# Kernel tuning notes

Measured on AMD Instinct MI355X. Metric: run time of the kernel, lower is better.

Reference implementation:

```python
import jax, jax.numpy as jnp
import numpy as np

B = 64
L_IN = 4001
L_CONV = 998  # (4001-10)//4 + 1
D = 1000
EPS = 1e-5


def _convlin(x, cw, cb, lw, lb):
    # x: (B,1,4001), cw: (1,1,10), lw: (1000,998)
    y = jax.lax.conv_general_dilated(
        x, cw, window_strides=(4,), padding='VALID',
        dimension_numbers=('NCH', 'OIH', 'NCH')) + cb[None, :, None]  # (B,1,998)
    y = y @ lw.T + lb  # (B,1,1000)
    return jax.nn.relu(y)


def setup_inputs() -> dict:
    key = jax.random.key(0)
    ks = jax.random.split(key, 24)
    f32 = jnp.float32
    inp = {
        'x': jax.random.normal(ks[0], (B, 1, L_IN), dtype=f32),
        'bn_gamma': jnp.ones((L_IN,), f32),
        'bn_beta': jnp.zeros((L_IN,), f32),
        'bn_mean': jax.random.normal(ks[1], (L_IN,), f32) * 0.1,
        'bn_var': jax.random.uniform(ks[2], (L_IN,), f32, 0.5, 1.5),
        'conv_w_q': jax.random.normal(ks[3], (1, 1, 10), f32) * 0.3,
        'conv_b_q': jax.random.normal(ks[4], (1,), f32) * 0.1,
        'lin_w_q': jax.random.normal(ks[5], (D, L_CONV), f32) * (1.0 / np.sqrt(L_CONV)),
        'lin_b_q': jax.random.normal(ks[6], (D,), f32) * 0.02,
        'conv_w_k': jax.random.normal(ks[7], (1, 1, 10), f32) * 0.3,
        'conv_b_k': jax.random.normal(ks[8], (1,), f32) * 0.1,
        'lin_w_k': jax.random.normal(ks[9], (D, L_CONV), f32) * (1.0 / np.sqrt(L_CONV)),
        'lin_b_k': jax.random.normal(ks[10], (D,), f32) * 0.02,
        'conv_w_v': jax.random.normal(ks[11], (1, 1, 10), f32) * 0.3,
        'conv_b_v': jax.random.normal(ks[12], (1,), f32) * 0.1,
        'lin_w_v': jax.random.normal(ks[13], (D, L_CONV), f32) * (1.0 / np.sqrt(L_CONV)),
        'lin_b_v': jax.random.normal(ks[14], (D,), f32) * 0.02,
        'in_proj_w': jax.random.normal(ks[15], (3, 1), f32),
        'in_proj_b': jax.random.normal(ks[16], (3,), f32) * 0.02,
        'out_proj_w': jax.random.normal(ks[17], (1, 1), f32),
        'out_proj_b': jax.random.normal(ks[18], (1,), f32) * 0.02,
        'out_w': jax.random.normal(ks[19], (D, D), f32) * (1.0 / np.sqrt(D)),
        'out_b': jax.random.normal(ks[20], (D,), f32) * 0.02,
    }
    return inp


def reference(x, bn_gamma, bn_beta, bn_mean, bn_var,
              conv_w_q, conv_b_q, lin_w_q, lin_b_q,
              conv_w_k, conv_b_k, lin_w_k, lin_b_k,
              conv_w_v, conv_b_v, lin_w_v, lin_b_v,
              in_proj_w, in_proj_b, out_proj_w, out_proj_b,
              out_w, out_b):
    # BatchNorm1d over last dim (eval mode, running stats); x: (B,1,4001)
    xn = (x - bn_mean[None, None, :]) * jax.lax.rsqrt(bn_var[None, None, :] + EPS)
    xn = xn * bn_gamma[None, None, :] + bn_beta[None, None, :]

    Q = _convlin(xn, conv_w_q, conv_b_q, lin_w_q, lin_b_q)[:, 0, :]  # (B,1000)
    K = _convlin(xn, conv_w_k, conv_b_k, lin_w_k, lin_b_k)[:, 0, :]
    V = _convlin(xn, conv_w_v, conv_b_v, lin_w_v, lin_b_v)[:, 0, :]

    # MHA with embed_dim=1, num_heads=1 -> scalar in-projections, scale = 1
    q = Q * in_proj_w[0, 0] + in_proj_b[0]  # (B,1000)
    k = K * in_proj_w[1, 0] + in_proj_b[1]
    v = V * in_proj_w[2, 0] + in_proj_b[2]

    scores = q[:, :, None] * k[:, None, :]  # (B,1000,1000)
    attn = jax.nn.softmax(scores, axis=-1)
    ctx = jnp.einsum('bqk,bk->bq', attn, v)  # (B,1000)
    ctx = ctx * out_proj_w[0, 0] + out_proj_b[0]

    out = ctx[:, None, :] @ out_w.T + out_b  # (B,1,1000)
    return out
```

## Files before the change

### kernel.cpp

```cpp
#include <hip/hip_runtime.h>
#include <math.h>

#define NB 64
#define LIN 4001
#define LC 998
#define ND 1000
#define EPSBN 1e-5f

#define CK 96
#define NCH_LIN 11
#define NCH_OUT 11

#define OFF_CONVT 0u
#define OFF_PP    191616u
#define OFF_Q     2354304u
#define OFF_KV    2418304u
#define OFF_CF    2549376u
#define OFF_OP    2613376u

__global__ __launch_bounds__(256) void k_bnconv(
    const float* __restrict__ x,
    const float* __restrict__ g, const float* __restrict__ be,
    const float* __restrict__ mu, const float* __restrict__ va,
    const float* __restrict__ cwq, const float* __restrict__ cbq,
    const float* __restrict__ cwk, const float* __restrict__ cbk,
    const float* __restrict__ cwv, const float* __restrict__ cbv,
    float* __restrict__ convT)
{
    int j = blockIdx.x * 256 + threadIdx.x;
    int b = blockIdx.y;
    if (j >= LC) return;
    const float* xb = x + (size_t)b * LIN + 4 * j;
    float aq = 0.f, ak = 0.f, av = 0.f;
#pragma unroll
    for (int t = 0; t < 10; ++t) {
        int i = 4 * j + t;
        float s  = g[i] * rsqrtf(va[i] + EPSBN);
        float xn = (xb[t] - mu[i]) * s + be[i];
        aq = fmaf(xn, cwq[t], aq);
        ak = fmaf(xn, cwk[t], ak);
        av = fmaf(xn, cwv[t], av);
    }
    convT[((size_t)0 * LC + j) * 64 + b] = aq + cbq[0];
    convT[((size_t)1 * LC + j) * 64 + b] = ak + cbk[0];
    convT[((size_t)2 * LC + j) * 64 + b] = av + cbv[0];
}

__device__ __forceinline__ void gemm_tile(
    const float* __restrict__ Asrc,
    const float* __restrict__ Brow,
    int ldB, int dgb, int j0, int jc,
    float* __restrict__ Pt,
    float* lds)
{
    float* ldsC = lds;
    float* ldsW = lds + 6144;
    int tid  = threadIdx.x;
    int lane = tid & 63;
    int w    = tid >> 6;
    int b0   = (lane & 7) << 3;
    int d0   = (lane >> 3) << 3;

    {
        const float4* src = (const float4*)Asrc;
        float4* dst = (float4*)ldsC;
        for (int t = tid; t < jc * 16; t += 256) dst[t] = src[t];
    }
    for (int idx = tid; idx < 3072; idx += 256) {
        int dd = idx / 48, j2 = idx % 48;
        int dg = dgb + dd;
        float2 v = make_float2(0.f, 0.f);
        if (dg < ND && 2 * j2 < jc)
            v = *(const float2*)(Brow + (size_t)dg * ldB + j0 + 2 * j2);
        ldsW[dd * 97 + 2 * j2]     = v.x;
        ldsW[dd * 97 + 2 * j2 + 1] = v.y;
    }
    __syncthreads();

    float acc[8][8];
#pragma unroll
    for (int i = 0; i < 8; ++i)
#pragma unroll
        for (int jx = 0; jx < 8; ++jx) acc[i][jx] = 0.f;

    int js = (jc * w) >> 2;
    int je = (jc * (w + 1)) >> 2;
    for (int jj = js; jj < je; ++jj) {
        float4 c0 = *(const float4*)(ldsC + jj * 64 + b0);
        float4 c1 = *(const float4*)(ldsC + jj * 64 + b0 + 4);
        float cv[8] = {c0.x, c0.y, c0.z, c0.w, c1.x, c1.y, c1.z, c1.w};
        float wv[8];
#pragma unroll
        for (int r = 0; r < 8; ++r) wv[r] = ldsW[(d0 + r) * 97 + jj];
#pragma unroll
        for (int i = 0; i < 8; ++i)
#pragma unroll
            for (int jx = 0; jx < 8; ++jx)
                acc[i][jx] = fmaf(cv[i], wv[jx], acc[i][jx]);
    }
    __syncthreads();

    for (int p = 0; p < 2; ++p) {
        float* red = lds + w * 2304;
#pragma unroll
        for (int i = 0; i < 8; ++i)
            *(float4*)(red + (b0 + i) * 36 + (d0 >> 1)) =
                make_float4(acc[i][4*p], acc[i][4*p+1], acc[i][4*p+2], acc[i][4*p+3]);
        __syncthreads();
        for (int t = tid; t < 512; t += 256) {
            int bb = t >> 3, gg = t & 7;
            int o = bb * 36 + 4 * gg;
            float4 a0 = *(const float4*)(lds + o);
            float4 a1 = *(const float4*)(lds + 2304 + o);
            float4 a2 = *(const float4*)(lds + 4608 + o);
            float4 a3 = *(const float4*)(lds + 6912 + o);
            float4 s;
            s.x = a0.x + a1.x + a2.x + a3.x;
            s.y = a0.y + a1.y + a2.y + a3.y;
            s.z = a0.z + a1.z + a2.z + a3.z;
            s.w = a0.w + a1.w + a2.w + a3.w;
            *(float4*)(Pt + bb * 64 + 8 * gg + 4 * p) = s;
        }
        __syncthreads();
    }
}

__global__ __launch_bounds__(256) void k_lin(
    const float* __restrict__ convT,
    const float* __restrict__ lwq, const float* __restrict__ lwk,
    const float* __restrict__ lwv,
    float* __restrict__ Pp)
{
    __shared__ float lds[12352];
    int dgb   = blockIdx.x * 64;
    int which = blockIdx.y;
    int chunk = blockIdx.z;
    int j0 = chunk * CK;
    int jc = (LC - j0 < CK) ? (LC - j0) : CK;
    const float* lw = (which == 0) ? lwq : ((which == 1) ? lwk : lwv);
    const float* Asrc = convT + ((size_t)which * LC + j0) * 64;
    float* Pt = Pp + (((size_t)chunk * 3 + which) * 16 + blockIdx.x) * 4096;
    gemm_tile(Asrc, lw, LC, dgb, j0, jc, Pt, lds);
}

__global__ __launch_bounds__(256) void k_act(
    const float* __restrict__ Pp,
    const float* __restrict__ lbq, const float* __restrict__ lbk,
    const float* __restrict__ lbv,
    const float* __restrict__ ipw, const float* __restrict__ ipb,
    float* __restrict__ q, float* __restrict__ kv)
{
    int i = blockIdx.x * 256 + threadIdx.x;
    int b = blockIdx.y;
    if (i >= ND) return;
    int it = i >> 6, il = i & 63;
    float s0 = 0.f, s1 = 0.f, s2 = 0.f;
    for (int c = 0; c < NCH_LIN; ++c) {
        size_t base = (((size_t)c * 3) * 16 + it) * 4096 + (il | (b << 6));
        s0 += Pp[base];
        s1 += Pp[base + 16 * 4096];
        s2 += Pp[base + 32 * 4096];
    }
    float yq = fmaxf(s0 + lbq[i], 0.f) * ipw[0] + ipb[0];
    float yk = fmaxf(s1 + lbk[i], 0.f) * ipw[1] + ipb[1];
    float yv = fmaxf(s2 + lbv[i], 0.f) * ipw[2] + ipb[2];
    q[(size_t)b * ND + i] = yq;
    kv[(size_t)b * 2048 + 2 * i]     = yk;
    kv[(size_t)b * 2048 + 2 * i + 1] = yv;
}

__global__ __launch_bounds__(256) void k_attn(
    const float* __restrict__ q, const float* __restrict__ kv,
    const float* __restrict__ opw, const float* __restrict__ opb,
    float* __restrict__ cfT)
{
    __shared__ float ldsKV[2048];
    __shared__ float sden[256];
    __shared__ float snum[256];
    __shared__ float rmax[4];
    __shared__ float rmin[4];
    int tid = threadIdx.x;
    int b   = blockIdx.y;
    int w   = tid >> 6;
    int ii  = tid & 63;
    int i   = blockIdx.x * 64 + ii;

    {
        const float4* src = (const float4*)(kv + (size_t)b * 2048);
        float4* dst = (float4*)ldsKV;
        for (int t = tid; t < 512; t += 256) dst[t] = src[t];
    }
    __syncthreads();

    const float2* kv2 = (const float2*)ldsKV;
    float km = -INFINITY, kn = INFINITY;
    for (int idx = tid; idx < ND; idx += 256) {
        float2 f = kv2[idx];
        km = fmaxf(km, f.x);
        kn = fminf(kn, f.x);
    }
#pragma unroll
    for (int off = 1; off < 64; off <<= 1) {
        km = fmaxf(km, __shfl_xor(km, off));
        kn = fminf(kn, __shfl_xor(kn, off));
    }
    if (ii == 0) { rmax[w] = km; rmin[w] = kn; }
    __syncthreads();
    km = fmaxf(fmaxf(rmax[0], rmax[1]), fmaxf(rmax[2], rmax[3]));
    kn = fminf(fminf(rmin[0], rmin[1]), fminf(rmin[2], rmin[3]));

    float qi = (i < ND) ? q[(size_t)b * ND + i] : 0.f;
    float m  = (qi >= 0.f) ? qi * km : qi * kn;

    int jb = w * 250;
    float den = 0.f, num = 0.f;
#pragma unroll 2
    for (int jl = 0; jl < 250; ++jl) {
        float2 f = kv2[jb + jl];
        float e  = __expf(fmaf(qi, f.x, -m));
        den += e;
        num = fmaf(e, f.y, num);
    }
    sden[tid] = den;
    snum[tid] = num;
    __syncthreads();
    if (w == 0 && i < ND) {
        float dt = sden[ii] + sden[64 + ii] + sden[128 + ii] + sden[192 + ii];
        float nt = snum[ii] + snum[64 + ii] + snum[128 + ii] + snum[192 + ii];
        cfT[(size_t)i * 64 + b] = (nt / dt) * opw[0] + opb[0];
    }
}

__global__ __launch_bounds__(256) void k_out(
    const float* __restrict__ cfT, const float* __restrict__ W,
    float* __restrict__ Op)
{
    __shared__ float lds[12352];
    int egb   = blockIdx.x * 64;
    int chunk = blockIdx.y;
    int j0 = chunk * CK;
    int jc = (ND - j0 < CK) ? (ND - j0) : CK;
    const float* Asrc = cfT + (size_t)j0 * 64;
    float* Pt = Op + ((size_t)chunk * 16 + blockIdx.x) * 4096;
    gemm_tile(Asrc, W, ND, egb, j0, jc, Pt, lds);
}

__global__ __launch_bounds__(256) void k_fin(
    const float* __restrict__ Op, const float* __restrict__ outb,
    float* __restrict__ out)
{
    int e = blockIdx.x * 256 + threadIdx.x;
    int b = blockIdx.y;
    if (e >= ND) return;
    float s = outb[e];
    size_t cell = ((size_t)(e >> 6)) * 4096 + (b << 6) + (e & 63);
    for (int c = 0; c < NCH_OUT; ++c)
        s += Op[(size_t)c * 16 * 4096 + cell];
    out[(size_t)b * ND + e] = s;
}

extern "C" void kernel_launch(void* const* d_in, const int* in_sizes, int n_in,
                              void* d_out, int out_size, void* d_ws, size_t ws_size,
                              hipStream_t stream)
{
    const float* x    = (const float*)d_in[0];
    const float* g    = (const float*)d_in[1];
    const float* be   = (const float*)d_in[2];
    const float* mu   = (const float*)d_in[3];
    const float* va   = (const float*)d_in[4];
    const float* cwq  = (const float*)d_in[5];
    const float* cbq  = (const float*)d_in[6];
    const float* lwq  = (const float*)d_in[7];
    const float* lbq  = (const float*)d_in[8];
    const float* cwk  = (const float*)d_in[9];
    const float* cbk  = (const float*)d_in[10];
    const float* lwk  = (const float*)d_in[11];
    const float* lbk  = (const float*)d_in[12];
    const float* cwv  = (const float*)d_in[13];
    const float* cbv  = (const float*)d_in[14];
    const float* lwv  = (const float*)d_in[15];
    const float* lbv  = (const float*)d_in[16];
    const float* ipw  = (const float*)d_in[17];
    const float* ipb  = (const float*)d_in[18];
    const float* opw  = (const float*)d_in[19];
    const float* opb  = (const float*)d_in[20];
    const float* W    = (const float*)d_in[21];
    const float* outb = (const float*)d_in[22];

    float* ws    = (float*)d_ws;
    float* convT = ws + OFF_CONVT;
    float* Pp    = ws + OFF_PP;
    float* q     = ws + OFF_Q;
    float* kv    = ws + OFF_KV;
    float* cfT   = ws + OFF_CF;
    float* Op    = ws + OFF_OP;
    float* out   = (float*)d_out;

    k_bnconv<<<dim3(4, 64), 256, 0, stream>>>(x, g, be, mu, va,
                                              cwq, cbq, cwk, cbk, cwv, cbv, convT);
    k_lin  <<<dim3(16, 3, NCH_LIN), 256, 0, stream>>>(convT, lwq, lwk, lwv, Pp);
    k_act  <<<dim3(4, 64), 256, 0, stream>>>(Pp, lbq, lbk, lbv, ipw, ipb, q, kv);
    k_attn <<<dim3(16, 64), 256, 0, stream>>>(q, kv, opw, opb, cfT);
    k_out  <<<dim3(16, NCH_OUT), 256, 0, stream>>>(cfT, W, Op);
    k_fin  <<<dim3(4, 64), 256, 0, stream>>>(Op, outb, out);
}
```

Measured before the change: 166.3 us.

## Fuse split-K reduction and activation into attention kernel, two queries per thread

Removes the separate k_act kernel. The attention kernel now reduces the split-K partial sums for K, V and Q itself, applies bias, ReLU and the in-projection, and writes K/V into LDS. Each block handles 128 queries, two per thread, so each K/V load from LDS is reused twice. Pre-scaling K by log2(e) lets the loop use exp2f. This drops one launch and a global round trip, but the K/V reduction is now repeated by each of the 8 blocks per batch row.

```diff
diff --git a/kernel.cpp b/kernel.cpp
--- a/kernel.cpp
+++ b/kernel.cpp
@@ -13,10 +13,8 @@
 
 #define OFF_CONVT 0u
 #define OFF_PP    191616u
-#define OFF_Q     2354304u
-#define OFF_KV    2418304u
-#define OFF_CF    2549376u
-#define OFF_OP    2613376u
+#define OFF_CF    2354304u
+#define OFF_OP    2418304u
 
 __global__ __launch_bounds__(256) void k_bnconv(
     const float* __restrict__ x,
@@ -143,91 +141,101 @@
     gemm_tile(Asrc, lw, LC, dgb, j0, jc, Pt, lds);
 }
 
-__global__ __launch_bounds__(256) void k_act(
+__global__ __launch_bounds__(256) void k_attn(
     const float* __restrict__ Pp,
     const float* __restrict__ lbq, const float* __restrict__ lbk,
     const float* __restrict__ lbv,
     const float* __restrict__ ipw, const float* __restrict__ ipb,
-    float* __restrict__ q, float* __restrict__ kv)
-{
-    int i = blockIdx.x * 256 + threadIdx.x;
-    int b = blockIdx.y;
-    if (i >= ND) return;
-    int it = i >> 6, il = i & 63;
-    float s0 = 0.f, s1 = 0.f, s2 = 0.f;
-    for (int c = 0; c < NCH_LIN; ++c) {
-        size_t base = (((size_t)c * 3) * 16 + it) * 4096 + (il | (b << 6));
-        s0 += Pp[base];
-        s1 += Pp[base + 16 * 4096];
-        s2 += Pp[base + 32 * 4096];
-    }
-    float yq = fmaxf(s0 + lbq[i], 0.f) * ipw[0] + ipb[0];
-    float yk = fmaxf(s1 + lbk[i], 0.f) * ipw[1] + ipb[1];
-    float yv = fmaxf(s2 + lbv[i], 0.f) * ipw[2] + ipb[2];
-    q[(size_t)b * ND + i] = yq;
-    kv[(size_t)b * 2048 + 2 * i]     = yk;
-    kv[(size_t)b * 2048 + 2 * i + 1] = yv;
-}
-
-__global__ __launch_bounds__(256) void k_attn(
-    const float* __restrict__ q, const float* __restrict__ kv,
     const float* __restrict__ opw, const float* __restrict__ opb,
     float* __restrict__ cfT)
 {
-    __shared__ float ldsKV[2048];
-    __shared__ float sden[256];
-    __shared__ float snum[256];
+    __shared__ float skv[2000];
+    __shared__ float sql[128];
+    __shared__ float sd[512];
+    __shared__ float sn[512];
     __shared__ float rmax[4];
     __shared__ float rmin[4];
-    int tid = threadIdx.x;
-    int b   = blockIdx.y;
-    int w   = tid >> 6;
-    int ii  = tid & 63;
-    int i   = blockIdx.x * 64 + ii;
-
-    {
-        const float4* src = (const float4*)(kv + (size_t)b * 2048);
-        float4* dst = (float4*)ldsKV;
-        for (int t = tid; t < 512; t += 256) dst[t] = src[t];
-    }
-    __syncthreads();
-
-    const float2* kv2 = (const float2*)ldsKV;
+    const float LOG2E = 1.4426950408889634f;
+    int tid  = threadIdx.x;
+    int b    = blockIdx.y;
+    int i0   = blockIdx.x * 128;
+    int w    = tid >> 6;
+    int lane = tid & 63;
+
+    float ipw1 = ipw[1], ipb1 = ipb[1];
+    float ipw2 = ipw[2], ipb2 = ipb[2];
+
+    for (int j = tid; j < ND; j += 256) {
+        int it = j >> 6, il = j & 63;
+        size_t base = ((size_t)it) * 4096 + (b << 6) + il;
+        float sk = 0.f, sv = 0.f;
+        for (int c = 0; c < NCH_LIN; ++c) {
+            sk += Pp[((size_t)(c * 3 + 1) * 16) * 4096 + base];
+            sv += Pp[((size_t)(c * 3 + 2) * 16) * 4096 + base];
+        }
+        float yk = fmaxf(sk + lbk[j], 0.f) * ipw1 + ipb1;
+        float yv = fmaxf(sv + lbv[j], 0.f) * ipw2 + ipb2;
+        skv[2 * j]     = yk * LOG2E;
+        skv[2 * j + 1] = yv;
+    }
+    if (tid < 128) {
+        int i = i0 + tid;
+        float sq = 0.f;
+        if (i < ND) {
+            int it = i >> 6, il = i & 63;
+            size_t base = ((size_t)it) * 4096 + (b << 6) + il;
+            for (int c = 0; c < NCH_LIN; ++c)
+                sq += Pp[((size_t)(c * 3 + 0) * 16) * 4096 + base];
+            sq = fmaxf(sq + lbq[i], 0.f) * ipw[0] + ipb[0];
+        }
+        sql[tid] = sq;
+    }
+    __syncthreads();
+
     float km = -INFINITY, kn = INFINITY;
-    for (int idx = tid; idx < ND; idx += 256) {
-        float2 f = kv2[idx];
-        km = fmaxf(km, f.x);
-        kn = fminf(kn, f.x);
+    for (int j = tid; j < ND; j += 256) {
+        float f = skv[2 * j];
+        km = fmaxf(km, f);
+        kn = fminf(kn, f);
     }
 #pragma unroll
     for (int off = 1; off < 64; off <<= 1) {
         km = fmaxf(km, __shfl_xor(km, off));
         kn = fminf(kn, __shfl_xor(kn, off));
     }
-    if (ii == 0) { rmax[w] = km; rmin[w] = kn; }
+    if (lane == 0) { rmax[w] = km; rmin[w] = kn; }
     __syncthreads();
     km = fmaxf(fmaxf(rmax[0], rmax[1]), fmaxf(rmax[2], rmax[3]));
     kn = fminf(fminf(rmin[0], rmin[1]), fminf(rmin[2], rmin[3]));
 
-    float qi = (i < ND) ? q[(size_t)b * ND + i] : 0.f;
-    float m  = (qi >= 0.f) ? qi * km : qi * kn;
-
+    float q0 = sql[lane];
+    float q1 = sql[64 + lane];
+    float m0 = (q0 >= 0.f) ? q0 * km : q0 * kn;
+    float m1 = (q1 >= 0.f) ? q1 * km : q1 * kn;
+    const float2* kv2 = (const float2*)skv;
     int jb = w * 250;
-    float den = 0.f, num = 0.f;
+    float d0a = 0.f, n0a = 0.f, d1a = 0.f, n1a = 0.f;
 #pragma unroll 2
     for (int jl = 0; jl < 250; ++jl) {
         float2 f = kv2[jb + jl];
-        float e  = __expf(fmaf(qi, f.x, -m));
-        den += e;
-        num = fmaf(e, f.y, num);
-    }
-    sden[tid] = den;
-    snum[tid] = num;
-    __syncthreads();
-    if (w == 0 && i < ND) {
-        float dt = sden[ii] + sden[64 + ii] + sden[128 + ii] + sden[192 + ii];
-        float nt = snum[ii] + snum[64 + ii] + snum[128 + ii] + snum[192 + ii];
-        cfT[(size_t)i * 64 + b] = (nt / dt) * opw[0] + opb[0];
+        float e0 = exp2f(fmaf(q0, f.x, -m0));
+        float e1 = exp2f(fmaf(q1, f.x, -m1));
+        d0a += e0; n0a = fmaf(e0, f.y, n0a);
+        d1a += e1; n1a = fmaf(e1, f.y, n1a);
+    }
+    sd[w * 128 + lane]      = d0a;
+    sd[w * 128 + 64 + lane] = d1a;
+    sn[w * 128 + lane]      = n0a;
+    sn[w * 128 + 64 + lane] = n1a;
+    __syncthreads();
+
+    if (tid < 128) {
+        int i = i0 + tid;
+        if (i < ND) {
+            float dt = sd[tid] + sd[128 + tid] + sd[256 + tid] + sd[384 + tid];
+            float nt = sn[tid] + sn[128 + tid] + sn[256 + tid] + sn[384 + tid];
+            cfT[(size_t)i * 64 + b] = (nt / dt) * opw[0] + opb[0];
+        }
     }
 }
 
@@ -290,8 +298,6 @@
     float* ws    = (float*)d_ws;
     float* convT = ws + OFF_CONVT;
     float* Pp    = ws + OFF_PP;
-    float* q     = ws + OFF_Q;
-    float* kv    = ws + OFF_KV;
     float* cfT   = ws + OFF_CF;
     float* Op    = ws + OFF_OP;
     float* out   = (float*)d_out;
@@ -299,8 +305,8 @@
     k_bnconv<<<dim3(4, 64), 256, 0, stream>>>(x, g, be, mu, va,
                                               cwq, cbq, cwk, cbk, cwv, cbv, convT);
     k_lin  <<<dim3(16, 3, NCH_LIN), 256, 0, stream>>>(convT, lwq, lwk, lwv, Pp);
-    k_act  <<<dim3(4, 64), 256, 0, stream>>>(Pp, lbq, lbk, lbv, ipw, ipb, q, kv);
-    k_attn <<<dim3(16, 64), 256, 0, stream>>>(q, kv, opw, opb, cfT);
+    k_attn <<<dim3(8, 64), 256, 0, stream>>>(Pp, lbq, lbk, lbv, ipw, ipb,
+                                             opw, opb, cfT);
     k_out  <<<dim3(16, NCH_OUT), 256, 0, stream>>>(cfT, W, Op);
     k_fin  <<<dim3(4, 64), 256, 0, stream>>>(Op, outb, out);
 }
```

New measurement: 174.5 us. 4.9% more time.

## Stream GEMM operands from global memory and retile K chunks with padded conv buffer

Applied to the files above, without the earlier changes.

Both linear GEMMs (the Q/K/V projections and the output projection) drop LDS staging of the convolution activations and weight tiles. Each thread now reads its 8 weight rows as float2 and its activations as float4 straight from global memory. The convT buffer is padded to 1024 zero-filled columns, and the K-chunk sizes change to 128 and 64, with a 3-blocks-per-CU occupancy hint. The softmax switches to exp2f with log2(e) folded into K during activation. Removing the row guard on weight loads means tail blocks read past the last weight row, which risks out-of-bounds access. Per-thread global loads also rely on the cache hierarchy for reuse.

```diff
diff --git a/kernel.cpp b/kernel.cpp
--- a/kernel.cpp
+++ b/kernel.cpp
@@ -7,16 +7,18 @@
 #define ND 1000
 #define EPSBN 1e-5f
 
-#define CK 96
-#define NCH_LIN 11
-#define NCH_OUT 11
+#define KP 1024
+#define CKL 128
+#define NCH_LIN 8
+#define CKO 64
+#define NCH_OUT 16
 
 #define OFF_CONVT 0u
-#define OFF_PP    191616u
-#define OFF_Q     2354304u
-#define OFF_KV    2418304u
-#define OFF_CF    2549376u
-#define OFF_OP    2613376u
+#define OFF_PP    196608u
+#define OFF_Q     1769472u
+#define OFF_KV    1833472u
+#define OFF_CF    1964544u
+#define OFF_OP    2030080u
 
 __global__ __launch_bounds__(256) void k_bnconv(
     const float* __restrict__ x,
@@ -29,77 +31,29 @@
 {
     int j = blockIdx.x * 256 + threadIdx.x;
     int b = blockIdx.y;
-    if (j >= LC) return;
-    const float* xb = x + (size_t)b * LIN + 4 * j;
     float aq = 0.f, ak = 0.f, av = 0.f;
-#pragma unroll
-    for (int t = 0; t < 10; ++t) {
-        int i = 4 * j + t;
-        float s  = g[i] * rsqrtf(va[i] + EPSBN);
-        float xn = (xb[t] - mu[i]) * s + be[i];
-        aq = fmaf(xn, cwq[t], aq);
-        ak = fmaf(xn, cwk[t], ak);
-        av = fmaf(xn, cwv[t], av);
-    }
-    convT[((size_t)0 * LC + j) * 64 + b] = aq + cbq[0];
-    convT[((size_t)1 * LC + j) * 64 + b] = ak + cbk[0];
-    convT[((size_t)2 * LC + j) * 64 + b] = av + cbv[0];
-}
-
-__device__ __forceinline__ void gemm_tile(
-    const float* __restrict__ Asrc,
-    const float* __restrict__ Brow,
-    int ldB, int dgb, int j0, int jc,
-    float* __restrict__ Pt,
-    float* lds)
-{
-    float* ldsC = lds;
-    float* ldsW = lds + 6144;
-    int tid  = threadIdx.x;
-    int lane = tid & 63;
-    int w    = tid >> 6;
-    int b0   = (lane & 7) << 3;
-    int d0   = (lane >> 3) << 3;
-
-    {
-        const float4* src = (const float4*)Asrc;
-        float4* dst = (float4*)ldsC;
-        for (int t = tid; t < jc * 16; t += 256) dst[t] = src[t];
-    }
-    for (int idx = tid; idx < 3072; idx += 256) {
-        int dd = idx / 48, j2 = idx % 48;
-        int dg = dgb + dd;
-        float2 v = make_float2(0.f, 0.f);
-        if (dg < ND && 2 * j2 < jc)
-            v = *(const float2*)(Brow + (size_t)dg * ldB + j0 + 2 * j2);
-        ldsW[dd * 97 + 2 * j2]     = v.x;
-        ldsW[dd * 97 + 2 * j2 + 1] = v.y;
-    }
-    __syncthreads();
-
-    float acc[8][8];
-#pragma unroll
-    for (int i = 0; i < 8; ++i)
-#pragma unroll
-        for (int jx = 0; jx < 8; ++jx) acc[i][jx] = 0.f;
-
-    int js = (jc * w) >> 2;
-    int je = (jc * (w + 1)) >> 2;
-    for (int jj = js; jj < je; ++jj) {
-        float4 c0 = *(const float4*)(ldsC + jj * 64 + b0);
-        float4 c1 = *(const float4*)(ldsC + jj * 64 + b0 + 4);
-        float cv[8] = {c0.x, c0.y, c0.z, c0.w, c1.x, c1.y, c1.z, c1.w};
-        float wv[8];
-#pragma unroll
-        for (int r = 0; r < 8; ++r) wv[r] = ldsW[(d0 + r) * 97 + jj];
-#pragma unroll
-        for (int i = 0; i < 8; ++i)
-#pragma unroll
-            for (int jx = 0; jx < 8; ++jx)
-                acc[i][jx] = fmaf(cv[i], wv[jx], acc[i][jx]);
-    }
-    __syncthreads();
-
+    if (j < LC) {
+        const float* xb = x + (size_t)b * LIN + 4 * j;
+#pragma unroll
+        for (int t = 0; t < 10; ++t) {
+            int i = 4 * j + t;
+            float s  = g[i] * rsqrtf(va[i] + EPSBN);
+            float xn = (xb[t] - mu[i]) * s + be[i];
+            aq = fmaf(xn, cwq[t], aq);
+            ak = fmaf(xn, cwk[t], ak);
+            av = fmaf(xn, cwv[t], av);
+        }
+        aq += cbq[0]; ak += cbk[0]; av += cbv[0];
+    }
+    convT[((size_t)0 * KP + j) * 64 + b] = aq;
+    convT[((size_t)1 * KP + j) * 64 + b] = ak;
+    convT[((size_t)2 * KP + j) * 64 + b] = av;
+}
+
+__device__ __forceinline__ void reduce_store(
+    float acc[8][8], float* lds, float* __restrict__ Pt,
+    int tid, int w, int b0, int d0)
+{
     for (int p = 0; p < 2; ++p) {
         float* red = lds + w * 2304;
 #pragma unroll
@@ -125,22 +79,75 @@
     }
 }
 
-__global__ __launch_bounds__(256) void k_lin(
+__device__ __forceinline__ void stream_mm(
+    float acc[8][8], const float* __restrict__ Cb,
+    const float* __restrict__ Wb, int ldB,
+    int j0, int jls, int nj, int jmax)
+{
+    for (int g2 = 0; g2 < (nj >> 1); ++g2) {
+        int jl = jls + 2 * g2;
+        int jg = j0 + jl;
+        float2 w2[8];
+        if (jg + 2 <= jmax) {
+#pragma unroll
+            for (int r = 0; r < 8; ++r)
+                w2[r] = *(const float2*)(Wb + (size_t)r * ldB + jl);
+        } else {
+#pragma unroll
+            for (int r = 0; r < 8; ++r) {
+                w2[r].x = (jg     < jmax) ? Wb[(size_t)r * ldB + jl]     : 0.f;
+                w2[r].y = (jg + 1 < jmax) ? Wb[(size_t)r * ldB + jl + 1] : 0.f;
+            }
+        }
+#pragma unroll
+        for (int u = 0; u < 2; ++u) {
+            const float* cp = Cb + (size_t)(jl + u) * 64;
+            float4 c0 = *(const float4*)(cp);
+            float4 c1 = *(const float4*)(cp + 4);
+            float cv[8] = {c0.x, c0.y, c0.z, c0.w, c1.x, c1.y, c1.z, c1.w};
+#pragma unroll
+            for (int i = 0; i < 8; ++i) {
+#pragma unroll
+                for (int jx = 0; jx < 8; ++jx) {
+                    float wv = u ? w2[jx].y : w2[jx].x;
+                    acc[i][jx] = fmaf(cv[i], wv, acc[i][jx]);
+                }
+            }
+        }
+    }
+}
+
+__global__ __launch_bounds__(256, 3) void k_lin(
     const float* __restrict__ convT,
     const float* __restrict__ lwq, const float* __restrict__ lwk,
     const float* __restrict__ lwv,
     float* __restrict__ Pp)
 {
-    __shared__ float lds[12352];
+    __shared__ float lds[9216];
+    int tid  = threadIdx.x;
+    int lane = tid & 63;
+    int w    = tid >> 6;
+    int b0   = (lane & 7) << 3;
+    int d0   = (lane >> 3) << 3;
     int dgb   = blockIdx.x * 64;
     int which = blockIdx.y;
     int chunk = blockIdx.z;
-    int j0 = chunk * CK;
-    int jc = (LC - j0 < CK) ? (LC - j0) : CK;
+    int j0 = chunk * CKL;
     const float* lw = (which == 0) ? lwq : ((which == 1) ? lwk : lwv);
-    const float* Asrc = convT + ((size_t)which * LC + j0) * 64;
+    const float* Cb = convT + ((size_t)which * KP + j0) * 64 + b0;
+    const float* Wb = lw + (size_t)(dgb + d0) * LC + j0;
+
+    float acc[8][8];
+#pragma unroll
+    for (int i = 0; i < 8; ++i)
+#pragma unroll
+        for (int jx = 0; jx < 8; ++jx) acc[i][jx] = 0.f;
+
+    stream_mm(acc, Cb, Wb, LC, j0, w * 32, 32, LC);
+
+    __syncthreads();
     float* Pt = Pp + (((size_t)chunk * 3 + which) * 16 + blockIdx.x) * 4096;
-    gemm_tile(Asrc, lw, LC, dgb, j0, jc, Pt, lds);
+    reduce_store(acc, lds, Pt, tid, w, b0, d0);
 }
 
 __global__ __launch_bounds__(256) void k_act(
@@ -161,11 +168,12 @@
         s1 += Pp[base + 16 * 4096];
         s2 += Pp[base + 32 * 4096];
     }
+    const float LOG2E = 1.4426950408889634f;
     float yq = fmaxf(s0 + lbq[i], 0.f) * ipw[0] + ipb[0];
     float yk = fmaxf(s1 + lbk[i], 0.f) * ipw[1] + ipb[1];
     float yv = fmaxf(s2 + lbv[i], 0.f) * ipw[2] + ipb[2];
     q[(size_t)b * ND + i] = yq;
-    kv[(size_t)b * 2048 + 2 * i]     = yk;
+    kv[(size_t)b * 2048 + 2 * i]     = yk * LOG2E;
     kv[(size_t)b * 2048 + 2 * i + 1] = yv;
 }
 
@@ -188,16 +196,16 @@
     {
         const float4* src = (const float4*)(kv + (size_t)b * 2048);
         float4* dst = (float4*)ldsKV;
-        for (int t = tid; t < 512; t += 256) dst[t] = src[t];
+        for (int t = tid; t < 500; t += 256) dst[t] = src[t];
     }
     __syncthreads();
 
     const float2* kv2 = (const float2*)ldsKV;
     float km = -INFINITY, kn = INFINITY;
     for (int idx = tid; idx < ND; idx += 256) {
-        float2 f = kv2[idx];
-        km = fmaxf(km, f.x);
-        kn = fminf(kn, f.x);
+        float f = ldsKV[2 * idx];
+        km = fmaxf(km, f);
+        kn = fminf(kn, f);
     }
 #pragma unroll
     for (int off = 1; off < 64; off <<= 1) {
@@ -217,32 +225,48 @@
 #pragma unroll 2
     for (int jl = 0; jl < 250; ++jl) {
         float2 f = kv2[jb + jl];
-        float e  = __expf(fmaf(qi, f.x, -m));
+        float e  = exp2f(fmaf(qi, f.x, -m));
         den += e;
         num = fmaf(e, f.y, num);
     }
     sden[tid] = den;
     snum[tid] = num;
     __syncthreads();
-    if (w == 0 && i < ND) {
+    if (w == 0) {
         float dt = sden[ii] + sden[64 + ii] + sden[128 + ii] + sden[192 + ii];
         float nt = snum[ii] + snum[64 + ii] + snum[128 + ii] + snum[192 + ii];
-        cfT[(size_t)i * 64 + b] = (nt / dt) * opw[0] + opb[0];
-    }
-}
-
-__global__ __launch_bounds__(256) void k_out(
+        float v  = (i < ND) ? (nt / dt) * opw[0] + opb[0] : 0.f;
+        cfT[(size_t)i * 64 + b] = v;
+    }
+}
+
+__global__ __launch_bounds__(256, 3) void k_out(
     const float* __restrict__ cfT, const float* __restrict__ W,
     float* __restrict__ Op)
 {
-    __shared__ float lds[12352];
+    __shared__ float lds[9216];
+    int tid  = threadIdx.x;
+    int lane = tid & 63;
+    int w    = tid >> 6;
+    int b0   = (lane & 7) << 3;
+    int d0   = (lane >> 3) << 3;
     int egb   = blockIdx.x * 64;
     int chunk = blockIdx.y;
-    int j0 = chunk * CK;
-    int jc = (ND - j0 < CK) ? (ND - j0) : CK;
-    const float* Asrc = cfT + (size_t)j0 * 64;
+    int j0 = chunk * CKO;
+    const float* Cb = cfT + (size_t)j0 * 64 + b0;
+    const float* Wb = W + (size_t)(egb + d0) * ND + j0;
+
+    float acc[8][8];
+#pragma unroll
+    for (int i = 0; i < 8; ++i)
+#pragma unroll
+        for (int jx = 0; jx < 8; ++jx) acc[i][jx] = 0.f;
+
+    stream_mm(acc, Cb, Wb, ND, j0, w * 16, 16, ND);
+
+    __syncthreads();
     float* Pt = Op + ((size_t)chunk * 16 + blockIdx.x) * 4096;
-    gemm_tile(Asrc, W, ND, egb, j0, jc, Pt, lds);
+    reduce_store(acc, lds, Pt, tid, w, b0, d0);
 }
 
 __global__ __launch_bounds__(256) void k_fin(
```

New measurement: 173.5 us. +4.3%, slower.
